# Optimization experiments

Measured on AMD Instinct MI355X. Metric: run time of the kernel, lower is better.

The kernel has to match this reference:

```python
import jax, jax.numpy as jnp
import numpy as np

B, NQ, NK, D = 64, 1024, 1024, 128
MASK_VALUE = -1e6


def setup_inputs() -> dict:
    key = jax.random.key(0)
    kq, kk, kv, kl = jax.random.split(key, 4)
    queries = jax.random.normal(kq, (B, NQ, D), dtype=jnp.float32)
    keys = jax.random.normal(kk, (B, NK, D), dtype=jnp.float32)
    values = jax.random.normal(kv, (B, NK, D), dtype=jnp.float32)
    valid_lens = jax.random.randint(kl, (B,), 1, NK + 1, dtype=jnp.int32)
    return {"queries": queries, "keys": keys, "values": values, "valid_lens": valid_lens}


def reference(queries, keys, values, valid_lens):
    d = queries.shape[-1]
    # scores: [B, Nq, Nk]
    scores = jnp.einsum("bqd,bkd->bqk", queries, keys) / jnp.sqrt(jnp.float32(d))
    # valid_lens [B] -> mask over last (key) axis, same for every query row
    key_pos = jnp.arange(scores.shape[-1])  # [Nk]
    mask = key_pos[None, None, :] < valid_lens[:, None, None]  # [B,1,Nk] broadcast
    scores = jnp.where(mask, scores, jnp.float32(MASK_VALUE))
    attn = jax.nn.softmax(scores, axis=-1)
    # dropout p=0.0 (eval): identity
    return jnp.einsum("bqk,bkd->bqd", attn, values)
```

## Files before the change

### kernel.cpp

```cpp
#include <hip/hip_runtime.h>

typedef __bf16 bf16x8 __attribute__((ext_vector_type(8)));
typedef __bf16 bf16x4 __attribute__((ext_vector_type(4)));
typedef __bf16 bf16x2 __attribute__((ext_vector_type(2)));
typedef float f32x4 __attribute__((ext_vector_type(4)));
typedef int i32x4 __attribute__((ext_vector_type(4)));

namespace {
constexpr int kNQ = 1024;
constexpr int kNK = 1024;
constexpr int kD = 128;
constexpr int kBQ = 64;
constexpr int kBK = 32;
constexpr int kKStride = 136;
constexpr int kVStride = 32;
constexpr float kScaleLog2e = 0.12751742f;
}

__device__ __forceinline__ int packbf(float a, float b) {
    bf16x2 t; t[0] = (__bf16)a; t[1] = (__bf16)b;
    return __builtin_bit_cast(int, t);
}

__global__ void lpt_sort(const int* __restrict__ VL, int* __restrict__ perm) {
    const int t = threadIdx.x;
    const int v = VL[t];
    int rank = 0;
    for (int j = 0; j < 64; ++j) {
        const int vj = VL[j];
        rank += (vj > v) || (vj == v && j < t);
    }
    perm[rank] = t;
}

__global__ __launch_bounds__(256, 4)
void fa_fwd(const float* __restrict__ Q, const float* __restrict__ K,
            const float* __restrict__ V, const int* __restrict__ VL,
            const int* __restrict__ perm, float* __restrict__ O)
{
    __shared__ __align__(16) __bf16 kls[2][kBK * kKStride];
    __shared__ __align__(16) __bf16 vls[2][kD * kVStride];

    const int tid  = threadIdx.x;
    const int wave = tid >> 6;
    const int lane = tid & 63;
    const int quad = lane >> 4;
    const int c16  = lane & 15;

    const int i = blockIdx.x;
    const int g = i >> 8;
    const int j = i & 255;
    int rank;
    if      (g == 0) rank = j;
    else if (g == 1) rank = 511 - j;
    else if (g == 2) rank = 512 + j;
    else             rank = 1023 - j;

    const int b    = perm[rank >> 4];
    const int qblk = rank & 15;
    const int q0   = qblk * kBQ + wave * 16;

    const int valid  = VL[b];
    const int ntiles = (valid + kBK - 1) / kBK;

    bf16x8 qf[4];
    {
        const float* qp = Q + ((size_t)b * kNQ + q0 + c16) * kD + quad * 8;
        #pragma unroll
        for (int f = 0; f < 4; ++f) {
            #pragma unroll
            for (int jj = 0; jj < 8; ++jj) qf[f][jj] = (__bf16)qp[f * 32 + jj];
        }
    }

    bf16x8 ones;
    #pragma unroll
    for (int jj = 0; jj < 8; ++jj) ones[jj] = (__bf16)1.0f;

    f32x4 acc[9];
    #pragma unroll
    for (int f = 0; f < 9; ++f) {
        acc[f][0] = 0.f; acc[f][1] = 0.f; acc[f][2] = 0.f; acc[f][3] = 0.f;
    }

    const int ksrow = tid >> 3;
    const int kscol = (tid & 7) * 16;
    const int vkg   = (tid & 7) * 4;
    const int vdb   = (tid >> 3) * 4;

    f32x4 kr[4], vr[4];

    auto load_regs = [&](int kbase) {
        const float* kp = K + ((size_t)b * kNK + kbase + ksrow) * kD + kscol;
        #pragma unroll
        for (int ii = 0; ii < 4; ++ii) kr[ii] = *(const f32x4*)(kp + ii * 4);
        const float* vp = V + ((size_t)b * kNK + kbase + vkg) * kD + vdb;
        #pragma unroll
        for (int ii = 0; ii < 4; ++ii) vr[ii] = *(const f32x4*)(vp + (size_t)ii * kD);
    };

    auto cvt_write = [&](int bufi) {
        bf16x8 kh;
        #pragma unroll
        for (int jj = 0; jj < 8; ++jj) kh[jj] = (__bf16)kr[jj >> 2][jj & 3];
        *(bf16x8*)&kls[bufi][ksrow * kKStride + kscol] = kh;
        #pragma unroll
        for (int jj = 0; jj < 8; ++jj) kh[jj] = (__bf16)kr[2 + (jj >> 2)][jj & 3];
        *(bf16x8*)&kls[bufi][ksrow * kKStride + kscol + 8] = kh;
        #pragma unroll
        for (int jj = 0; jj < 4; ++jj) {
            bf16x4 vh;
            #pragma unroll
            for (int ii = 0; ii < 4; ++ii) vh[ii] = (__bf16)vr[ii][jj];
            *(bf16x4*)&vls[bufi][(vdb + jj) * kVStride + vkg] = vh;
        }
    };

    const int a0 = ((quad & 1) << 7) + (c16 << 2);
    const int a1 = a0 + 64;

    load_regs(0);
    cvt_write(0);
    __syncthreads();

    int cur = 0;
    for (int t = 0; t < ntiles; ++t) {
        const int kb = t * kBK;
        const bool more = (t + 1 < ntiles);
        if (more) load_regs(kb + kBK);

        f32x4 s0a = {0.f,0.f,0.f,0.f}, s0b = {0.f,0.f,0.f,0.f};
        f32x4 s1a = {0.f,0.f,0.f,0.f}, s1b = {0.f,0.f,0.f,0.f};
        const __bf16* kbuf = kls[cur];
        #pragma unroll
        for (int f = 0; f < 2; ++f) {
            bf16x8 kf = *(const bf16x8*)&kbuf[c16 * kKStride + f * 32 + quad * 8];
            s0a = __builtin_amdgcn_mfma_f32_16x16x32_bf16(kf, qf[f], s0a, 0, 0, 0);
        }
        #pragma unroll
        for (int f = 2; f < 4; ++f) {
            bf16x8 kf = *(const bf16x8*)&kbuf[c16 * kKStride + f * 32 + quad * 8];
            s0b = __builtin_amdgcn_mfma_f32_16x16x32_bf16(kf, qf[f], s0b, 0, 0, 0);
        }
        #pragma unroll
        for (int f = 0; f < 2; ++f) {
            bf16x8 kf = *(const bf16x8*)&kbuf[(16 + c16) * kKStride + f * 32 + quad * 8];
            s1a = __builtin_amdgcn_mfma_f32_16x16x32_bf16(kf, qf[f], s1a, 0, 0, 0);
        }
        #pragma unroll
        for (int f = 2; f < 4; ++f) {
            bf16x8 kf = *(const bf16x8*)&kbuf[(16 + c16) * kKStride + f * 32 + quad * 8];
            s1b = __builtin_amdgcn_mfma_f32_16x16x32_bf16(kf, qf[f], s1b, 0, 0, 0);
        }
        f32x4 s0 = s0a + s0b;
        f32x4 s1 = s1a + s1b;

        if (kb + kBK > valid) {
            #pragma unroll
            for (int r = 0; r < 4; ++r) {
                if (kb + quad * 4 + r >= valid)      s0[r] = -1e30f;
                if (kb + 16 + quad * 4 + r >= valid) s1[r] = -1e30f;
            }
        }

        #pragma unroll
        for (int r = 0; r < 4; ++r) {
            s0[r] = exp2f(s0[r] * kScaleLog2e);
            s1[r] = exp2f(s1[r] * kScaleLog2e);
        }

        const int pp01 = packbf(s0[0], s0[1]), pp23 = packbf(s0[2], s0[3]);
        const int qq01 = packbf(s1[0], s1[1]), qq23 = packbf(s1[2], s1[3]);
        const int b0p = __builtin_amdgcn_ds_bpermute(a0, pp01);
        const int b0q = __builtin_amdgcn_ds_bpermute(a0, qq01);
        const int b1p = __builtin_amdgcn_ds_bpermute(a0, pp23);
        const int b1q = __builtin_amdgcn_ds_bpermute(a0, qq23);
        const int b2p = __builtin_amdgcn_ds_bpermute(a1, pp01);
        const int b2q = __builtin_amdgcn_ds_bpermute(a1, qq01);
        const int b3p = __builtin_amdgcn_ds_bpermute(a1, pp23);
        const int b3q = __builtin_amdgcn_ds_bpermute(a1, qq23);
        const bool lo = quad < 2;
        i32x4 pd;
        pd[0] = lo ? b0p : b0q;
        pd[1] = lo ? b1p : b1q;
        pd[2] = lo ? b2p : b2q;
        pd[3] = lo ? b3p : b3q;
        const bf16x8 pf = __builtin_bit_cast(bf16x8, pd);

        if (more) cvt_write(cur ^ 1);

        const __bf16* vbuf = vls[cur];
        #pragma unroll
        for (int f = 0; f < 8; ++f) {
            const bf16x8 vf = *(const bf16x8*)&vbuf[(f * 16 + c16) * kVStride + quad * 8];
            acc[f] = __builtin_amdgcn_mfma_f32_16x16x32_bf16(pf, vf, acc[f], 0, 0, 0);
        }
        acc[8] = __builtin_amdgcn_mfma_f32_16x16x32_bf16(pf, ones, acc[8], 0, 0, 0);

        __syncthreads();
        cur ^= 1;
    }

    float* ob = O + ((size_t)b * kNQ + q0) * kD;
    #pragma unroll
    for (int r = 0; r < 4; ++r) {
        const float inv = 1.0f / acc[8][r];
        #pragma unroll
        for (int f = 0; f < 8; ++f) {
            ob[(quad * 4 + r) * kD + f * 16 + c16] = acc[f][r] * inv;
        }
    }
}

extern "C" void kernel_launch(void* const* d_in, const int* in_sizes, int n_in,
                              void* d_out, int out_size, void* d_ws, size_t ws_size,
                              hipStream_t stream) {
    const float* Q = (const float*)d_in[0];
    const float* K = (const float*)d_in[1];
    const float* V = (const float*)d_in[2];
    const int*  VL = (const int*)d_in[3];
    float* O = (float*)d_out;
    int* perm = (int*)d_ws;
    lpt_sort<<<1, 64, 0, stream>>>(VL, perm);
    fa_fwd<<<dim3(1024), 256, 0, stream>>>(Q, K, V, VL, perm, O);
}
```

Baseline: 179.9 us.

## Double query rows per block so each K/V tile feeds two MFMA groups

Each wave now handles 32 query rows instead of 16, giving 128 rows per block and 512 blocks in place of 1024. Every K/V tile staged to LDS is therefore reused across twice as many queries, halving global K/V traffic and bf16 conversion work per query. The block ordering is simplified to a two-pass snake over the sorted batches. Smaller changes swap in the hardware exp2 builtin and advance the K/V pointers incrementally. The cost is twice the accumulator registers, with launch bounds lowered to 2 blocks per SM, and fewer blocks for load balancing.

After: 177.2 us. No clear change (-1.5%).

```diff
diff --git a/kernel.cpp b/kernel.cpp
--- a/kernel.cpp
+++ b/kernel.cpp
@@ -10,10 +10,11 @@
 constexpr int kNQ = 1024;
 constexpr int kNK = 1024;
 constexpr int kD = 128;
-constexpr int kBQ = 64;
+constexpr int kBQ = 128;
 constexpr int kBK = 32;
 constexpr int kKStride = 136;
 constexpr int kVStride = 32;
+constexpr int kItems = 512;
 constexpr float kScaleLog2e = 0.12751742f;
 }
 
@@ -33,7 +34,7 @@
     perm[rank] = t;
 }
 
-__global__ __launch_bounds__(256, 4)
+__global__ __launch_bounds__(256, 2)
 void fa_fwd(const float* __restrict__ Q, const float* __restrict__ K,
             const float* __restrict__ V, const int* __restrict__ VL,
             const int* __restrict__ perm, float* __restrict__ O)
@@ -48,28 +49,23 @@
     const int c16  = lane & 15;
 
     const int i = blockIdx.x;
-    const int g = i >> 8;
-    const int j = i & 255;
-    int rank;
-    if      (g == 0) rank = j;
-    else if (g == 1) rank = 511 - j;
-    else if (g == 2) rank = 512 + j;
-    else             rank = 1023 - j;
-
-    const int b    = perm[rank >> 4];
-    const int qblk = rank & 15;
-    const int q0   = qblk * kBQ + wave * 16;
+    const int rank = (i < 256) ? i : 767 - i;
+
+    const int b    = perm[rank >> 3];
+    const int qblk = rank & 7;
+    const int q0   = qblk * kBQ + wave * 32;
 
     const int valid  = VL[b];
     const int ntiles = (valid + kBK - 1) / kBK;
 
-    bf16x8 qf[4];
-    {
-        const float* qp = Q + ((size_t)b * kNQ + q0 + c16) * kD + quad * 8;
+    bf16x8 qf[2][4];
+    #pragma unroll
+    for (int g = 0; g < 2; ++g) {
+        const float* qp = Q + ((size_t)b * kNQ + q0 + g * 16 + c16) * kD + quad * 8;
         #pragma unroll
         for (int f = 0; f < 4; ++f) {
             #pragma unroll
-            for (int jj = 0; jj < 8; ++jj) qf[f][jj] = (__bf16)qp[f * 32 + jj];
+            for (int jj = 0; jj < 8; ++jj) qf[g][f][jj] = (__bf16)qp[f * 32 + jj];
         }
     }
 
@@ -77,26 +73,32 @@
     #pragma unroll
     for (int jj = 0; jj < 8; ++jj) ones[jj] = (__bf16)1.0f;
 
-    f32x4 acc[9];
-    #pragma unroll
-    for (int f = 0; f < 9; ++f) {
-        acc[f][0] = 0.f; acc[f][1] = 0.f; acc[f][2] = 0.f; acc[f][3] = 0.f;
-    }
+    f32x4 acc[2][9];
+    #pragma unroll
+    for (int g = 0; g < 2; ++g)
+        #pragma unroll
+        for (int f = 0; f < 9; ++f) {
+            acc[g][f][0] = 0.f; acc[g][f][1] = 0.f;
+            acc[g][f][2] = 0.f; acc[g][f][3] = 0.f;
+        }
 
     const int ksrow = tid >> 3;
     const int kscol = (tid & 7) * 16;
     const int vkg   = (tid & 7) * 4;
     const int vdb   = (tid >> 3) * 4;
 
+    const float* kp = K + ((size_t)b * kNK + ksrow) * kD + kscol;
+    const float* vp = V + ((size_t)b * kNK + vkg) * kD + vdb;
+
     f32x4 kr[4], vr[4];
 
-    auto load_regs = [&](int kbase) {
-        const float* kp = K + ((size_t)b * kNK + kbase + ksrow) * kD + kscol;
+    auto load_regs = [&]() {
         #pragma unroll
         for (int ii = 0; ii < 4; ++ii) kr[ii] = *(const f32x4*)(kp + ii * 4);
-        const float* vp = V + ((size_t)b * kNK + kbase + vkg) * kD + vdb;
         #pragma unroll
         for (int ii = 0; ii < 4; ++ii) vr[ii] = *(const f32x4*)(vp + (size_t)ii * kD);
+        kp += kBK * kD;
+        vp += kBK * kD;
     };
 
     auto cvt_write = [&](int bufi) {
@@ -118,74 +120,71 @@
 
     const int a0 = ((quad & 1) << 7) + (c16 << 2);
     const int a1 = a0 + 64;
-
-    load_regs(0);
-    cvt_write(0);
-    __syncthreads();
-
-    int cur = 0;
-    for (int t = 0; t < ntiles; ++t) {
-        const int kb = t * kBK;
-        const bool more = (t + 1 < ntiles);
-        if (more) load_regs(kb + kBK);
-
-        f32x4 s0a = {0.f,0.f,0.f,0.f}, s0b = {0.f,0.f,0.f,0.f};
-        f32x4 s1a = {0.f,0.f,0.f,0.f}, s1b = {0.f,0.f,0.f,0.f};
-        const __bf16* kbuf = kls[cur];
-        #pragma unroll
-        for (int f = 0; f < 2; ++f) {
-            bf16x8 kf = *(const bf16x8*)&kbuf[c16 * kKStride + f * 32 + quad * 8];
-            s0a = __builtin_amdgcn_mfma_f32_16x16x32_bf16(kf, qf[f], s0a, 0, 0, 0);
-        }
-        #pragma unroll
-        for (int f = 2; f < 4; ++f) {
-            bf16x8 kf = *(const bf16x8*)&kbuf[c16 * kKStride + f * 32 + quad * 8];
-            s0b = __builtin_amdgcn_mfma_f32_16x16x32_bf16(kf, qf[f], s0b, 0, 0, 0);
-        }
-        #pragma unroll
-        for (int f = 0; f < 2; ++f) {
-            bf16x8 kf = *(const bf16x8*)&kbuf[(16 + c16) * kKStride + f * 32 + quad * 8];
-            s1a = __builtin_amdgcn_mfma_f32_16x16x32_bf16(kf, qf[f], s1a, 0, 0, 0);
-        }
-        #pragma unroll
-        for (int f = 2; f < 4; ++f) {
-            bf16x8 kf = *(const bf16x8*)&kbuf[(16 + c16) * kKStride + f * 32 + quad * 8];
-            s1b = __builtin_amdgcn_mfma_f32_16x16x32_bf16(kf, qf[f], s1b, 0, 0, 0);
-        }
-        f32x4 s0 = s0a + s0b;
-        f32x4 s1 = s1a + s1b;
-
-        if (kb + kBK > valid) {
-            #pragma unroll
-            for (int r = 0; r < 4; ++r) {
-                if (kb + quad * 4 + r >= valid)      s0[r] = -1e30f;
-                if (kb + 16 + quad * 4 + r >= valid) s1[r] = -1e30f;
-            }
-        }
-
-        #pragma unroll
-        for (int r = 0; r < 4; ++r) {
-            s0[r] = exp2f(s0[r] * kScaleLog2e);
-            s1[r] = exp2f(s1[r] * kScaleLog2e);
-        }
-
-        const int pp01 = packbf(s0[0], s0[1]), pp23 = packbf(s0[2], s0[3]);
-        const int qq01 = packbf(s1[0], s1[1]), qq23 = packbf(s1[2], s1[3]);
-        const int b0p = __builtin_amdgcn_ds_bpermute(a0, pp01);
-        const int b0q = __builtin_amdgcn_ds_bpermute(a0, qq01);
-        const int b1p = __builtin_amdgcn_ds_bpermute(a0, pp23);
-        const int b1q = __builtin_amdgcn_ds_bpermute(a0, qq23);
-        const int b2p = __builtin_amdgcn_ds_bpermute(a1, pp01);
-        const int b2q = __builtin_amdgcn_ds_bpermute(a1, qq01);
-        const int b3p = __builtin_amdgcn_ds_bpermute(a1, pp23);
-        const int b3q = __builtin_amdgcn_ds_bpermute(a1, qq23);
-        const bool lo = quad < 2;
+    const bool lo = quad < 2;
+
+    auto cToA = [&](const f32x4& sA, const f32x4& sB) -> bf16x8 {
+        const int p01 = packbf(sA[0], sA[1]), p23 = packbf(sA[2], sA[3]);
+        const int q01 = packbf(sB[0], sB[1]), q23 = packbf(sB[2], sB[3]);
+        const int b0p = __builtin_amdgcn_ds_bpermute(a0, p01);
+        const int b0q = __builtin_amdgcn_ds_bpermute(a0, q01);
+        const int b1p = __builtin_amdgcn_ds_bpermute(a0, p23);
+        const int b1q = __builtin_amdgcn_ds_bpermute(a0, q23);
+        const int b2p = __builtin_amdgcn_ds_bpermute(a1, p01);
+        const int b2q = __builtin_amdgcn_ds_bpermute(a1, q01);
+        const int b3p = __builtin_amdgcn_ds_bpermute(a1, p23);
+        const int b3q = __builtin_amdgcn_ds_bpermute(a1, q23);
         i32x4 pd;
         pd[0] = lo ? b0p : b0q;
         pd[1] = lo ? b1p : b1q;
         pd[2] = lo ? b2p : b2q;
         pd[3] = lo ? b3p : b3q;
-        const bf16x8 pf = __builtin_bit_cast(bf16x8, pd);
+        return __builtin_bit_cast(bf16x8, pd);
+    };
+
+    load_regs();
+    cvt_write(0);
+    __syncthreads();
+
+    int cur = 0;
+    for (int t = 0; t < ntiles; ++t) {
+        const int kb = t * kBK;
+        const bool more = (t + 1 < ntiles);
+        if (more) load_regs();
+
+        f32x4 s00 = {0.f,0.f,0.f,0.f}, s01 = {0.f,0.f,0.f,0.f};
+        f32x4 s10 = {0.f,0.f,0.f,0.f}, s11 = {0.f,0.f,0.f,0.f};
+        const __bf16* kbuf = kls[cur];
+        #pragma unroll
+        for (int f = 0; f < 4; ++f) {
+            bf16x8 kf = *(const bf16x8*)&kbuf[c16 * kKStride + f * 32 + quad * 8];
+            s00 = __builtin_amdgcn_mfma_f32_16x16x32_bf16(kf, qf[0][f], s00, 0, 0, 0);
+            s01 = __builtin_amdgcn_mfma_f32_16x16x32_bf16(kf, qf[1][f], s01, 0, 0, 0);
+        }
+        #pragma unroll
+        for (int f = 0; f < 4; ++f) {
+            bf16x8 kf = *(const bf16x8*)&kbuf[(16 + c16) * kKStride + f * 32 + quad * 8];
+            s10 = __builtin_amdgcn_mfma_f32_16x16x32_bf16(kf, qf[0][f], s10, 0, 0, 0);
+            s11 = __builtin_amdgcn_mfma_f32_16x16x32_bf16(kf, qf[1][f], s11, 0, 0, 0);
+        }
+
+        if (kb + kBK > valid) {
+            #pragma unroll
+            for (int r = 0; r < 4; ++r) {
+                if (kb + quad * 4 + r >= valid)      { s00[r] = -1e30f; s01[r] = -1e30f; }
+                if (kb + 16 + quad * 4 + r >= valid) { s10[r] = -1e30f; s11[r] = -1e30f; }
+            }
+        }
+
+        #pragma unroll
+        for (int r = 0; r < 4; ++r) {
+            s00[r] = __builtin_amdgcn_exp2f(s00[r] * kScaleLog2e);
+            s01[r] = __builtin_amdgcn_exp2f(s01[r] * kScaleLog2e);
+            s10[r] = __builtin_amdgcn_exp2f(s10[r] * kScaleLog2e);
+            s11[r] = __builtin_amdgcn_exp2f(s11[r] * kScaleLog2e);
+        }
+
+        const bf16x8 pf0 = cToA(s00, s10);
+        const bf16x8 pf1 = cToA(s01, s11);
 
         if (more) cvt_write(cur ^ 1);
 
@@ -193,9 +192,11 @@
         #pragma unroll
         for (int f = 0; f < 8; ++f) {
             const bf16x8 vf = *(const bf16x8*)&vbuf[(f * 16 + c16) * kVStride + quad * 8];
-            acc[f] = __builtin_amdgcn_mfma_f32_16x16x32_bf16(pf, vf, acc[f], 0, 0, 0);
-        }
-        acc[8] = __builtin_amdgcn_mfma_f32_16x16x32_bf16(pf, ones, acc[8], 0, 0, 0);
+            acc[0][f] = __builtin_amdgcn_mfma_f32_16x16x32_bf16(pf0, vf, acc[0][f], 0, 0, 0);
+            acc[1][f] = __builtin_amdgcn_mfma_f32_16x16x32_bf16(pf1, vf, acc[1][f], 0, 0, 0);
+        }
+        acc[0][8] = __builtin_amdgcn_mfma_f32_16x16x32_bf16(pf0, ones, acc[0][8], 0, 0, 0);
+        acc[1][8] = __builtin_amdgcn_mfma_f32_16x16x32_bf16(pf1, ones, acc[1][8], 0, 0, 0);
 
         __syncthreads();
         cur ^= 1;
@@ -203,11 +204,14 @@
 
     float* ob = O + ((size_t)b * kNQ + q0) * kD;
     #pragma unroll
-    for (int r = 0; r < 4; ++r) {
-        const float inv = 1.0f / acc[8][r];
-        #pragma unroll
-        for (int f = 0; f < 8; ++f) {
-            ob[(quad * 4 + r) * kD + f * 16 + c16] = acc[f][r] * inv;
+    for (int g = 0; g < 2; ++g) {
+        #pragma unroll
+        for (int r = 0; r < 4; ++r) {
+            const float inv = 1.0f / acc[g][8][r];
+            #pragma unroll
+            for (int f = 0; f < 8; ++f) {
+                ob[(g * 16 + quad * 4 + r) * kD + f * 16 + c16] = acc[g][f][r] * inv;
+            }
         }
     }
 }
@@ -222,5 +226,5 @@
     float* O = (float*)d_out;
     int* perm = (int*)d_ws;
     lpt_sort<<<1, 64, 0, stream>>>(VL, perm);
-    fa_fwd<<<dim3(1024), 256, 0, stream>>>(Q, K, V, VL, perm, O);
-}
+    fa_fwd<<<dim3(kItems), 256, 0, stream>>>(Q, K, V, VL, perm, O);
+}
```
